# Kernel optimization log

Hardware: AMD Instinct MI355X
Metric: run time of the kernel (lower is better)

Reference implementation:

```python
import jax, jax.numpy as jnp
import numpy as np


def postorder_positions(depth):
    """Post-order index of each node in a perfect binary tree of given depth.
    Returns dict: level -> np.array of post-order indices for the left-to-right
    nodes at that level (level 0 = leaves, level `depth` = root)."""
    levels = {0: np.array([0], dtype=np.int64)}
    size = 1  # size of depth-(d-1) subtree
    for d in range(1, depth + 1):
        new = {l: np.concatenate([levels[l], levels[l] + size]) for l in range(d)}
        new[d] = np.array([2 * size], dtype=np.int64)
        levels = new
        size = 2 * size + 1
    return levels


def setup_inputs() -> dict:
    key = jax.random.key(0)
    k1, k2, k3, k4, k5, k6 = jax.random.split(key, 6)
    VOCAB, E, LBL, LEAVES = 50000, 100, 2, 131072  # 2**17 leaves
    word_ids = jax.random.randint(k1, (LEAVES,), 0, VOCAB, dtype=jnp.int32)
    emb_table = jax.random.normal(k2, (VOCAB, E), dtype=jnp.float32) * 0.1
    Wl = jax.random.normal(k3, (E, E), dtype=jnp.float32) * 0.1
    bl = jax.random.normal(k4, (E,), dtype=jnp.float32) * 0.1
    Wp = jax.random.normal(k5, (LBL, E), dtype=jnp.float32) * 0.1
    bp = jax.random.normal(k6, (LBL,), dtype=jnp.float32) * 0.1
    return {"word_ids": word_ids, "emb_table": emb_table, "Wl": Wl, "bl": bl, "Wp": Wp, "bp": bp}


def reference(word_ids, emb_table, Wl, bl, Wp, bp):
    # Perfect binary tree, batched level-by-level (same math as the per-node
    # Python recursion in the torch module). NOTE: original uses fcl for BOTH
    # children, so internal node = relu(fcl(left) + fcl(right)).
    L = word_ids.shape[0]
    D = int(round(np.log2(L)))
    pos = postorder_positions(D)
    n_nodes = 2 * L - 1

    h = emb_table[word_ids]  # [L, E] leaf states
    out = jnp.zeros((n_nodes, 1, bp.shape[0]), dtype=h.dtype)
    for lvl in range(D + 1):
        proj = h @ Wp.T + bp                     # [n_lvl, label]
        out = out.at[jnp.asarray(pos[lvl])].set(proj[:, None, :])
        if lvl < D:
            # fcl(left)+fcl(right) = (left+right) @ Wl^T + 2*bl, then relu
            h = jax.nn.relu((h[0::2] + h[1::2]) @ Wl.T + 2.0 * bl)
    return out  # [n_nodes, 1, label] in post-order, matching torch.cat(node_list)
```

## Files before the change

### kernel.cpp

```cpp
#include <hip/hip_runtime.h>

typedef _Float16 h8v __attribute__((ext_vector_type(8)));
typedef float f4v __attribute__((ext_vector_type(4)));

#define RS 136
#define SD 68

__device__ __forceinline__ unsigned pk2f(float a, float b) {
  unsigned short ha = __builtin_bit_cast(unsigned short, (_Float16)a);
  unsigned short hb = __builtin_bit_cast(unsigned short, (_Float16)b);
  return (unsigned)ha | ((unsigned)hb << 16);
}
__device__ __forceinline__ float2 upk(unsigned u) {
  _Float16 lo = __builtin_bit_cast(_Float16, (unsigned short)(u & 0xffffu));
  _Float16 hi = __builtin_bit_cast(_Float16, (unsigned short)(u >> 16));
  return make_float2((float)lo, (float)hi);
}

__global__ void prep_kernel(const float* __restrict__ Wl, const float* __restrict__ emb,
                            const float* __restrict__ Wp, const float* __restrict__ bp,
                            unsigned short* __restrict__ Wlf, unsigned* __restrict__ embh,
                            float2* __restrict__ pw, unsigned* __restrict__ cnts) {
  const long t = (long)blockIdx.x * 256 + threadIdx.x;
  if (t < 400000L) {
    const int w = (int)(t >> 3), q = (int)(t & 7);
    const float4* row4 = (const float4*)(emb + (size_t)w * 100);
    uint2* ed = (uint2*)(embh + (size_t)w * 64);
    float q0 = 0.f, q1 = 0.f;
    #pragma unroll
    for (int m = 0; m < 4; ++m) {
      int j = q + 8 * m;
      if (j < 25) {
        float4 v = row4[j];
        q0 = fmaf(v.x, Wp[4*j], fmaf(v.y, Wp[4*j+1],
             fmaf(v.z, Wp[4*j+2], fmaf(v.w, Wp[4*j+3], q0))));
        q1 = fmaf(v.x, Wp[100+4*j], fmaf(v.y, Wp[100+4*j+1],
             fmaf(v.z, Wp[100+4*j+2], fmaf(v.w, Wp[100+4*j+3], q1))));
        ed[j] = make_uint2(pk2f(v.x, v.y), pk2f(v.z, v.w));
      }
    }
    if (q < 7) ed[25 + q] = make_uint2(0u, 0u);
    q0 += __shfl_xor(q0, 1, 64); q0 += __shfl_xor(q0, 2, 64); q0 += __shfl_xor(q0, 4, 64);
    q1 += __shfl_xor(q1, 1, 64); q1 += __shfl_xor(q1, 2, 64); q1 += __shfl_xor(q1, 4, 64);
    if (q == 0) pw[w] = make_float2(q0 + bp[0], q1 + bp[1]);
  } else {
    long j = t - 400128L;
    if (j >= 0 && j < 128 * 128) {
      int o = (int)(j >> 7), k = (int)(j & 127);
      _Float16 v = (_Float16)0.f;
      if (o < 100 && k < 100) v = (_Float16)Wl[o * 100 + k];
      Wlf[j] = __builtin_bit_cast(unsigned short, v);
    }
    if (blockIdx.x == 1563 && threadIdx.x >= 192 && threadIdx.x < 224)
      cnts[threadIdx.x - 192] = 0u;
  }
}

__device__ __forceinline__ void load_bfrags(
    const unsigned short* __restrict__ Wlf, const float* __restrict__ bl,
    h8v (&B0)[4], h8v (&B1)[4], float& bias0, float& bias1,
    int wave, int quad, int c16) {
  int col0 = wave * 32 + c16;
  int col1 = col0 + 16;
  bias0 = (col0 < 100) ? 2.0f * bl[col0] : 0.f;
  bias1 = (col1 < 100) ? 2.0f * bl[col1] : 0.f;
  const _Float16* w0 = (const _Float16*)Wlf + col0 * 128 + quad * 8;
  const _Float16* w1 = (const _Float16*)Wlf + col1 * 128 + quad * 8;
  B0[0] = *(const h8v*)(w0);      B0[1] = *(const h8v*)(w0 + 32);
  B0[2] = *(const h8v*)(w0 + 64); B0[3] = *(const h8v*)(w0 + 96);
  B1[0] = *(const h8v*)(w1);      B1[1] = *(const h8v*)(w1 + 32);
  B1[2] = *(const h8v*)(w1 + 64); B1[3] = *(const h8v*)(w1 + 96);
}

__device__ __forceinline__ void mfma_level(
    const _Float16* srcE, const _Float16* srcO, bool pairMode,
    _Float16* dstE, _Float16* dstO, int nOut,
    const h8v (&B0)[4], const h8v (&B1)[4], float bias0, float bias1,
    int lane, int wave) {
  const int quad = lane >> 4, c16 = lane & 15;
  const int col0 = wave * 32 + c16, col1 = col0 + 16;
  const int tiles = (nOut + 15) >> 4;
  for (int rt = 0; rt < tiles; ++rt) {
    const int r = rt * 16 + c16;
    const h8v* pe = (const h8v*)(srcE + (size_t)r * RS + quad * 8);
    h8v A0, A1, A2, A3;
    if (pairMode) {
      const h8v* po = (const h8v*)(srcO + (size_t)r * RS + quad * 8);
      A0 = pe[0] + po[0];  A1 = pe[4] + po[4];
      A2 = pe[8] + po[8];  A3 = pe[12] + po[12];
    } else {
      A0 = pe[0]; A1 = pe[4]; A2 = pe[8]; A3 = pe[12];
    }
    f4v a0 = {bias0, bias0, bias0, bias0};
    f4v a1 = {bias1, bias1, bias1, bias1};
    a0 = __builtin_amdgcn_mfma_f32_16x16x32_f16(A0, B0[0], a0, 0, 0, 0);
    a0 = __builtin_amdgcn_mfma_f32_16x16x32_f16(A1, B0[1], a0, 0, 0, 0);
    a0 = __builtin_amdgcn_mfma_f32_16x16x32_f16(A2, B0[2], a0, 0, 0, 0);
    a0 = __builtin_amdgcn_mfma_f32_16x16x32_f16(A3, B0[3], a0, 0, 0, 0);
    a1 = __builtin_amdgcn_mfma_f32_16x16x32_f16(A0, B1[0], a1, 0, 0, 0);
    a1 = __builtin_amdgcn_mfma_f32_16x16x32_f16(A1, B1[1], a1, 0, 0, 0);
    a1 = __builtin_amdgcn_mfma_f32_16x16x32_f16(A2, B1[2], a1, 0, 0, 0);
    a1 = __builtin_amdgcn_mfma_f32_16x16x32_f16(A3, B1[3], a1, 0, 0, 0);
    #pragma unroll
    for (int rg = 0; rg < 4; ++rg) {
      int row = rt * 16 + quad * 4 + rg;
      _Float16* dr = ((row & 1) ? dstO : dstE) + (size_t)(row >> 1) * RS;
      dr[col0] = (_Float16)fmaxf(a0[rg], 0.f);
      dr[col1] = (_Float16)fmaxf(a1[rg], 0.f);
    }
  }
}

__device__ __forceinline__ void proj_rows(
    const _Float16* E, const _Float16* O, int nRows, const float* WpS,
    float bp0, float bp1, int lvl, long gbase, float* __restrict__ out, int tid) {
  if (tid >= nRows) return;
  const unsigned* row = (const unsigned*)((tid & 1) ? O : E) + (size_t)(tid >> 1) * SD;
  float q0 = bp0, q1 = bp1;
  #pragma unroll
  for (int p = 0; p < 25; ++p) {
    uint2 u = ((const uint2*)row)[p];
    float2 a = upk(u.x), b = upk(u.y);
    q0 = fmaf(a.x, WpS[4*p], fmaf(a.y, WpS[4*p+1],
         fmaf(b.x, WpS[4*p+2], fmaf(b.y, WpS[4*p+3], q0))));
    q1 = fmaf(a.x, WpS[128+4*p], fmaf(a.y, WpS[128+4*p+1],
         fmaf(b.x, WpS[128+4*p+2], fmaf(b.y, WpS[128+4*p+3], q1))));
  }
  long g = gbase + tid;
  long pos = ((g + 1) << (lvl + 1)) - 2 - __popc((unsigned)g);
  out[2 * pos] = q0; out[2 * pos + 1] = q1;
}

__device__ void tree_phase(
    const unsigned* __restrict__ src, unsigned* __restrict__ hdst,
    _Float16* Ea, _Float16* Oa, _Float16* Eb, _Float16* Ob,
    const float* WpS, float bp0, float bp1,
    const h8v (&B0)[4], const h8v (&B1)[4], float bias0, float bias1,
    float* __restrict__ out, int firstLvl, int nLvl, int nIn, int finalProj,
    long blk, int tid, int lane, int wave) {
  {
    unsigned* Ed = (unsigned*)Ea; unsigned* Od = (unsigned*)Oa;
    for (int i = tid; i < 64 * 64; i += 256) {
      int r = i >> 6, d = i & 63;
      unsigned val = (r < nIn && d < 50)
          ? __hip_atomic_load(&src[(size_t)r * 50 + d], __ATOMIC_RELAXED,
                              __HIP_MEMORY_SCOPE_AGENT)
          : 0u;
      ((r & 1) ? Od : Ed)[(r >> 1) * SD + d] = val;
    }
    unsigned* Ed2 = (unsigned*)Eb; unsigned* Od2 = (unsigned*)Ob;
    for (int i = tid; i < 32 * 64; i += 256) {
      int r = i >> 6, d = i & 63;
      ((r & 1) ? Od2 : Ed2)[(r >> 1) * SD + d] = 0u;
    }
  }
  __syncthreads();
  _Float16 *sE = Ea, *sO = Oa, *dE = Eb, *dO = Ob;
  int n = nIn >> 1;
  for (int p = 0; p < nLvl; ++p) {
    mfma_level(sE, sO, true, dE, dO, n, B0, B1, bias0, bias1, lane, wave);
    proj_rows(sE, sO, n * 2, WpS, bp0, bp1, firstLvl + p - 1,
              blk * (n * 2), out, tid);
    __syncthreads();
    _Float16* t;
    t = sE; sE = dE; dE = t;
    t = sO; sO = dO; dO = t;
    n >>= 1;
  }
  int R = nIn >> nLvl;
  if (finalProj)
    proj_rows(sE, sO, R, WpS, bp0, bp1, firstLvl + nLvl - 1, blk * R, out, tid);
  if (hdst) {
    for (int i = tid; i < R * 50; i += 256) {
      int r = i / 50, d = i % 50;
      unsigned val = ((const unsigned*)((r & 1) ? sO : sE))[(r >> 1) * SD + d];
      __hip_atomic_store(&hdst[(size_t)blk * R * 50 + i], val,
                         __ATOMIC_RELAXED, __HIP_MEMORY_SCOPE_AGENT);
    }
  }
  __syncthreads();
}

__global__ __launch_bounds__(256, 4) void mega_kernel(
    const int* __restrict__ word_ids, const unsigned* __restrict__ embh,
    const float2* __restrict__ pw,
    const unsigned short* __restrict__ Wlf, const float* __restrict__ bl,
    const float* __restrict__ Wp, const float* __restrict__ bp,
    unsigned* __restrict__ h7g, unsigned* __restrict__ h13g,
    unsigned* __restrict__ cnts, float* __restrict__ out) {
  __shared__ _Float16 S1[64 * RS];
  __shared__ _Float16 Ea[32 * RS], Oa[32 * RS];
  __shared__ float WpS[256];
  __shared__ int claimS;
  _Float16* const Eb = S1;
  _Float16* const Ob = S1 + 16 * RS;

  const int tid = threadIdx.x, lane = tid & 63;
  const int wave = __builtin_amdgcn_readfirstlane(tid >> 6);
  const int quad = lane >> 4, c16 = lane & 15;
  const int blk = blockIdx.x;

  {
    int r = tid >> 7, c = tid & 127;
    WpS[tid] = (c < 100) ? Wp[r * 100 + c] : 0.f;
  }
  const float bp0 = bp[0], bp1 = bp[1];

  const int l = tid >> 1, hh = tid & 1;
  const long gL = (long)blk * 128 + l;
  const int wid = word_ids[gL];
  const uint4* erow = (const uint4*)(embh + (size_t)wid * 64 + hh * 32);
  uint4 w4[8];
  #pragma unroll
  for (int i = 0; i < 8; ++i) w4[i] = erow[i];

  if (hh == 0) {
    float2 p = pw[wid];
    long pos = ((gL + 1) << 1) - 2 - __popc((unsigned)gL);
    out[2 * pos] = p.x; out[2 * pos + 1] = p.y;
  }

  {
    unsigned* S1d = (unsigned*)S1;
    const unsigned* wd = (const unsigned*)w4;
    #pragma unroll
    for (int k = 0; k < 32; ++k) {
      unsigned u = wd[k];
      unsigned us = __shfl_xor(u, 2, 64);
      float2 a = upk(u), b = upk(us);
      unsigned pk = pk2f(a.x + b.x, a.y + b.y);
      if ((tid & 2) == 0) S1d[(size_t)(tid >> 2) * SD + hh * 32 + k] = pk;
    }
  }
  h8v B0[4], B1[4]; float bias0, bias1;
  load_bfrags(Wlf, bl, B0, B1, bias0, bias1, wave, quad, c16);
  __syncthreads();

  mfma_level(S1, nullptr, false, Ea, Oa, 64, B0, B1, bias0, bias1, lane, wave);
  __syncthreads();
  mfma_level(Ea, Oa, true, Eb, Ob, 32, B0, B1, bias0, bias1, lane, wave);
  proj_rows(Ea, Oa, 64, WpS, bp0, bp1, 1, (long)blk * 64, out, tid);
  __syncthreads();
  mfma_level(Eb, Ob, true, Ea, Oa, 16, B0, B1, bias0, bias1, lane, wave);
  proj_rows(Eb, Ob, 32, WpS, bp0, bp1, 2, (long)blk * 32, out, tid);
  __syncthreads();
  mfma_level(Ea, Oa, true, Eb, Ob, 8, B0, B1, bias0, bias1, lane, wave);
  proj_rows(Ea, Oa, 16, WpS, bp0, bp1, 3, (long)blk * 16, out, tid);
  __syncthreads();
  mfma_level(Eb, Ob, true, Ea, Oa, 4, B0, B1, bias0, bias1, lane, wave);
  proj_rows(Eb, Ob, 8, WpS, bp0, bp1, 4, (long)blk * 8, out, tid);
  __syncthreads();
  mfma_level(Ea, Oa, true, Eb, Ob, 2, B0, B1, bias0, bias1, lane, wave);
  proj_rows(Ea, Oa, 4, WpS, bp0, bp1, 5, (long)blk * 4, out, tid);
  __syncthreads();
  mfma_level(Eb, Ob, true, Ea, Oa, 1, B0, B1, bias0, bias1, lane, wave);
  proj_rows(Eb, Ob, 2, WpS, bp0, bp1, 6, (long)blk * 2, out, tid);
  __syncthreads();
  if (tid < 50)
    __hip_atomic_store(&h7g[(size_t)blk * 50 + tid], ((unsigned*)Ea)[tid],
                       __ATOMIC_RELAXED, __HIP_MEMORY_SCOPE_AGENT);
  __syncthreads();

  const int g = blk >> 6;
  if (tid == 0) {
    unsigned old = __hip_atomic_fetch_add(&cnts[g], 1u, __ATOMIC_RELAXED,
                                          __HIP_MEMORY_SCOPE_AGENT);
    claimS = (old == 63u);
  }
  __syncthreads();
  if (!claimS) return;

  tree_phase(h7g + (size_t)g * 64 * 50, h13g, Ea, Oa, Eb, Ob, WpS, bp0, bp1,
             B0, B1, bias0, bias1, out, 8, 6, 64, 0, (long)g, tid, lane, wave);

  if (tid == 0) {
    unsigned old = __hip_atomic_fetch_add(&cnts[16], 1u, __ATOMIC_RELAXED,
                                          __HIP_MEMORY_SCOPE_AGENT);
    claimS = (old == 15u);
  }
  __syncthreads();
  if (!claimS) return;

  tree_phase(h13g, nullptr, Ea, Oa, Eb, Ob, WpS, bp0, bp1,
             B0, B1, bias0, bias1, out, 14, 4, 16, 1, 0L, tid, lane, wave);
}

extern "C" void kernel_launch(void* const* d_in, const int* in_sizes, int n_in,
                              void* d_out, int out_size, void* d_ws, size_t ws_size,
                              hipStream_t stream) {
  const int*   word_ids = (const int*)  d_in[0];
  const float* emb      = (const float*)d_in[1];
  const float* Wl       = (const float*)d_in[2];
  const float* bl       = (const float*)d_in[3];
  const float* Wp       = (const float*)d_in[4];
  const float* bp       = (const float*)d_in[5];
  float* out = (float*)d_out;

  unsigned*       embh = (unsigned*)d_ws;
  float2*         pw   = (float2*)((char*)d_ws + 12800000);
  unsigned short* Wlf  = (unsigned short*)((char*)d_ws + 13200000);
  unsigned*       h7g  = (unsigned*)((char*)d_ws + 13232768);
  unsigned*       h13g = (unsigned*)((char*)d_ws + 13437568);
  unsigned*       cnts = (unsigned*)((char*)d_ws + 13440768);

  prep_kernel<<<1627, 256, 0, stream>>>(Wl, emb, Wp, bp, Wlf, embh, pw, cnts);
  mega_kernel<<<1024, 256, 0, stream>>>(word_ids, embh, pw, Wlf, bl, Wp, bp,
                                        h7g, h13g, cnts, out);
}
```

Measured before the change: 145.4 us.

## Halve per-block leaves, shrink LDS row stride, double grid and occupancy

Each block now handles 64 leaves instead of 128, and the grid doubles to 2048 blocks. The fp16 row stride in shared memory drops from 136 to 104 halves, the embedding table stride from 64 to 56 dwords, and the Wp shared copy is removed in favour of direct global reads. Together these cut LDS per block enough for launch bounds of 8 blocks per CU, aiming to raise occupancy and latency hiding. The cross-block reduction tree is rebalanced to match: 32 groups of 64, then a final phase of 32 inputs over 5 levels. The cost is more counter atomics, and proj_rows now reads Wp from global or cache instead of LDS.

```diff
diff --git a/kernel.cpp b/kernel.cpp
--- a/kernel.cpp
+++ b/kernel.cpp
@@ -3,8 +3,10 @@
 typedef _Float16 h8v __attribute__((ext_vector_type(8)));
 typedef float f4v __attribute__((ext_vector_type(4)));
 
-#define RS 136
-#define SD 68
+#define RS 104
+#define SD 52
+#define LROWS 96
+#define LDS_DW (LROWS * SD + 16)
 
 __device__ __forceinline__ unsigned pk2f(float a, float b) {
   unsigned short ha = __builtin_bit_cast(unsigned short, (_Float16)a);
@@ -25,7 +27,7 @@
   if (t < 400000L) {
     const int w = (int)(t >> 3), q = (int)(t & 7);
     const float4* row4 = (const float4*)(emb + (size_t)w * 100);
-    uint2* ed = (uint2*)(embh + (size_t)w * 64);
+    uint2* ed = (uint2*)(embh + (size_t)w * 56);
     float q0 = 0.f, q1 = 0.f;
     #pragma unroll
     for (int m = 0; m < 4; ++m) {
@@ -39,7 +41,7 @@
         ed[j] = make_uint2(pk2f(v.x, v.y), pk2f(v.z, v.w));
       }
     }
-    if (q < 7) ed[25 + q] = make_uint2(0u, 0u);
+    if (q < 3) ed[25 + q] = make_uint2(0u, 0u);
     q0 += __shfl_xor(q0, 1, 64); q0 += __shfl_xor(q0, 2, 64); q0 += __shfl_xor(q0, 4, 64);
     q1 += __shfl_xor(q1, 1, 64); q1 += __shfl_xor(q1, 2, 64); q1 += __shfl_xor(q1, 4, 64);
     if (q == 0) pw[w] = make_float2(q0 + bp[0], q1 + bp[1]);
@@ -51,7 +53,7 @@
       if (o < 100 && k < 100) v = (_Float16)Wl[o * 100 + k];
       Wlf[j] = __builtin_bit_cast(unsigned short, v);
     }
-    if (blockIdx.x == 1563 && threadIdx.x >= 192 && threadIdx.x < 224)
+    if (blockIdx.x == 1563 && threadIdx.x >= 192 && threadIdx.x < 240)
       cnts[threadIdx.x - 192] = 0u;
   }
 }
@@ -105,14 +107,14 @@
     for (int rg = 0; rg < 4; ++rg) {
       int row = rt * 16 + quad * 4 + rg;
       _Float16* dr = ((row & 1) ? dstO : dstE) + (size_t)(row >> 1) * RS;
-      dr[col0] = (_Float16)fmaxf(a0[rg], 0.f);
-      dr[col1] = (_Float16)fmaxf(a1[rg], 0.f);
+      if (col0 < 104) dr[col0] = (_Float16)fmaxf(a0[rg], 0.f);
+      if (col1 < 104) dr[col1] = (_Float16)fmaxf(a1[rg], 0.f);
     }
   }
 }
 
 __device__ __forceinline__ void proj_rows(
-    const _Float16* E, const _Float16* O, int nRows, const float* WpS,
+    const _Float16* E, const _Float16* O, int nRows, const float* __restrict__ Wp,
     float bp0, float bp1, int lvl, long gbase, float* __restrict__ out, int tid) {
   if (tid >= nRows) return;
   const unsigned* row = (const unsigned*)((tid & 1) ? O : E) + (size_t)(tid >> 1) * SD;
@@ -121,10 +123,10 @@
   for (int p = 0; p < 25; ++p) {
     uint2 u = ((const uint2*)row)[p];
     float2 a = upk(u.x), b = upk(u.y);
-    q0 = fmaf(a.x, WpS[4*p], fmaf(a.y, WpS[4*p+1],
-         fmaf(b.x, WpS[4*p+2], fmaf(b.y, WpS[4*p+3], q0))));
-    q1 = fmaf(a.x, WpS[128+4*p], fmaf(a.y, WpS[128+4*p+1],
-         fmaf(b.x, WpS[128+4*p+2], fmaf(b.y, WpS[128+4*p+3], q1))));
+    q0 = fmaf(a.x, Wp[4*p], fmaf(a.y, Wp[4*p+1],
+         fmaf(b.x, Wp[4*p+2], fmaf(b.y, Wp[4*p+3], q0))));
+    q1 = fmaf(a.x, Wp[100+4*p], fmaf(a.y, Wp[100+4*p+1],
+         fmaf(b.x, Wp[100+4*p+2], fmaf(b.y, Wp[100+4*p+3], q1))));
   }
   long g = gbase + tid;
   long pos = ((g + 1) << (lvl + 1)) - 2 - __popc((unsigned)g);
@@ -133,34 +135,34 @@
 
 __device__ void tree_phase(
     const unsigned* __restrict__ src, unsigned* __restrict__ hdst,
-    _Float16* Ea, _Float16* Oa, _Float16* Eb, _Float16* Ob,
-    const float* WpS, float bp0, float bp1,
+    _Float16* TE, _Float16* TO, _Float16* Eb, _Float16* Ob,
+    const float* __restrict__ Wp, float bp0, float bp1,
     const h8v (&B0)[4], const h8v (&B1)[4], float bias0, float bias1,
     float* __restrict__ out, int firstLvl, int nLvl, int nIn, int finalProj,
-    long blk, int tid, int lane, int wave) {
+    long blkg, int tid, int lane, int wave) {
   {
-    unsigned* Ed = (unsigned*)Ea; unsigned* Od = (unsigned*)Oa;
-    for (int i = tid; i < 64 * 64; i += 256) {
-      int r = i >> 6, d = i & 63;
-      unsigned val = (r < nIn && d < 50)
-          ? __hip_atomic_load(&src[(size_t)r * 50 + d], __ATOMIC_RELAXED,
-                              __HIP_MEMORY_SCOPE_AGENT)
-          : 0u;
-      ((r & 1) ? Od : Ed)[(r >> 1) * SD + d] = val;
-    }
-    unsigned* Ed2 = (unsigned*)Eb; unsigned* Od2 = (unsigned*)Ob;
-    for (int i = tid; i < 32 * 64; i += 256) {
-      int r = i >> 6, d = i & 63;
-      ((r & 1) ? Od2 : Ed2)[(r >> 1) * SD + d] = 0u;
-    }
-  }
-  __syncthreads();
-  _Float16 *sE = Ea, *sO = Oa, *dE = Eb, *dO = Ob;
+    unsigned* Ed = (unsigned*)TE; unsigned* Od = (unsigned*)TO;
+    const int d = tid & 63;
+    if (d < SD) {
+      for (int r = tid >> 6; r < 64; r += 4) {
+        unsigned val = 0u;
+        if (r < nIn && d < 50)
+          val = __hip_atomic_load(&src[(size_t)r * 50 + d], __ATOMIC_RELAXED,
+                                  __HIP_MEMORY_SCOPE_AGENT);
+        ((r & 1) ? Od : Ed)[(r >> 1) * SD + d] = val;
+      }
+      unsigned* Ed2 = (unsigned*)Eb; unsigned* Od2 = (unsigned*)Ob;
+      for (int r = tid >> 6; r < 32; r += 4)
+        ((r & 1) ? Od2 : Ed2)[(r >> 1) * SD + d] = 0u;
+    }
+  }
+  __syncthreads();
+  _Float16 *sE = TE, *sO = TO, *dE = Eb, *dO = Ob;
   int n = nIn >> 1;
   for (int p = 0; p < nLvl; ++p) {
     mfma_level(sE, sO, true, dE, dO, n, B0, B1, bias0, bias1, lane, wave);
-    proj_rows(sE, sO, n * 2, WpS, bp0, bp1, firstLvl + p - 1,
-              blk * (n * 2), out, tid);
+    proj_rows(sE, sO, n * 2, Wp, bp0, bp1, firstLvl + p - 1,
+              blkg * (n * 2), out, tid);
     __syncthreads();
     _Float16* t;
     t = sE; sE = dE; dE = t;
@@ -169,95 +171,104 @@
   }
   int R = nIn >> nLvl;
   if (finalProj)
-    proj_rows(sE, sO, R, WpS, bp0, bp1, firstLvl + nLvl - 1, blk * R, out, tid);
+    proj_rows(sE, sO, R, Wp, bp0, bp1, firstLvl + nLvl - 1, blkg * R, out, tid);
   if (hdst) {
     for (int i = tid; i < R * 50; i += 256) {
-      int r = i / 50, d = i % 50;
-      unsigned val = ((const unsigned*)((r & 1) ? sO : sE))[(r >> 1) * SD + d];
-      __hip_atomic_store(&hdst[(size_t)blk * R * 50 + i], val,
+      int r = i / 50, d2 = i % 50;
+      unsigned val = ((const unsigned*)((r & 1) ? sO : sE))[(r >> 1) * SD + d2];
+      __hip_atomic_store(&hdst[(size_t)blkg * R * 50 + i], val,
                          __ATOMIC_RELAXED, __HIP_MEMORY_SCOPE_AGENT);
     }
   }
   __syncthreads();
 }
 
-__global__ __launch_bounds__(256, 4) void mega_kernel(
+__global__ __launch_bounds__(256, 8) void mega_kernel(
     const int* __restrict__ word_ids, const unsigned* __restrict__ embh,
     const float2* __restrict__ pw,
     const unsigned short* __restrict__ Wlf, const float* __restrict__ bl,
     const float* __restrict__ Wp, const float* __restrict__ bp,
-    unsigned* __restrict__ h7g, unsigned* __restrict__ h13g,
+    unsigned* __restrict__ h6g, unsigned* __restrict__ h12g,
     unsigned* __restrict__ cnts, float* __restrict__ out) {
-  __shared__ _Float16 S1[64 * RS];
-  __shared__ _Float16 Ea[32 * RS], Oa[32 * RS];
-  __shared__ float WpS[256];
+  __shared__ _Float16 LB[2 * LDS_DW];
   __shared__ int claimS;
-  _Float16* const Eb = S1;
-  _Float16* const Ob = S1 + 16 * RS;
+  _Float16* const S1 = LB;
+  _Float16* const Ea = LB + 32 * RS;
+  _Float16* const Oa = LB + 48 * RS;
+  _Float16* const Eb = LB + 64 * RS;
+  _Float16* const Ob = LB + 80 * RS;
 
   const int tid = threadIdx.x, lane = tid & 63;
   const int wave = __builtin_amdgcn_readfirstlane(tid >> 6);
   const int quad = lane >> 4, c16 = lane & 15;
   const int blk = blockIdx.x;
 
+  const int l4 = tid >> 2, q = tid & 3;
+  const int wid = word_ids[(size_t)blk * 64 + l4];
+  const uint4* erow = (const uint4*)(embh + (size_t)wid * 56);
+  uint4 w4[4];
+  #pragma unroll
+  for (int k = 0; k < 4; ++k) {
+    int c = q + 4 * k;
+    if (c < 14) w4[k] = erow[c];
+  }
+  float2 p0 = make_float2(0.f, 0.f);
+  if (tid < 64) p0 = pw[word_ids[(size_t)blk * 64 + tid]];
+  const float bp0 = bp[0], bp1 = bp[1];
+
   {
-    int r = tid >> 7, c = tid & 127;
-    WpS[tid] = (c < 100) ? Wp[r * 100 + c] : 0.f;
-  }
-  const float bp0 = bp[0], bp1 = bp[1];
-
-  const int l = tid >> 1, hh = tid & 1;
-  const long gL = (long)blk * 128 + l;
-  const int wid = word_ids[gL];
-  const uint4* erow = (const uint4*)(embh + (size_t)wid * 64 + hh * 32);
-  uint4 w4[8];
-  #pragma unroll
-  for (int i = 0; i < 8; ++i) w4[i] = erow[i];
-
-  if (hh == 0) {
-    float2 p = pw[wid];
-    long pos = ((gL + 1) << 1) - 2 - __popc((unsigned)gL);
-    out[2 * pos] = p.x; out[2 * pos + 1] = p.y;
-  }
+    unsigned* lb = (unsigned*)LB;
+    for (int i = tid; i < LDS_DW; i += 256) lb[i] = 0u;
+  }
+  __syncthreads();
 
   {
     unsigned* S1d = (unsigned*)S1;
-    const unsigned* wd = (const unsigned*)w4;
+    const int m = tid >> 3;
     #pragma unroll
-    for (int k = 0; k < 32; ++k) {
-      unsigned u = wd[k];
-      unsigned us = __shfl_xor(u, 2, 64);
-      float2 a = upk(u), b = upk(us);
-      unsigned pk = pk2f(a.x + b.x, a.y + b.y);
-      if ((tid & 2) == 0) S1d[(size_t)(tid >> 2) * SD + hh * 32 + k] = pk;
+    for (int k = 0; k < 4; ++k) {
+      int c = q + 4 * k;
+      if (c < 14) {
+        uint4 u = w4[k], s;
+        s.x = __shfl_xor(u.x, 4, 64); s.y = __shfl_xor(u.y, 4, 64);
+        s.z = __shfl_xor(u.z, 4, 64); s.w = __shfl_xor(u.w, 4, 64);
+        h8v hm = __builtin_bit_cast(h8v, u);
+        h8v hs = __builtin_bit_cast(h8v, s);
+        h8v sum = hm + hs;
+        if ((tid & 4) == 0 && c < 13)
+          *(uint4*)(S1d + (size_t)m * SD + c * 4) = __builtin_bit_cast(uint4, sum);
+      }
     }
   }
   h8v B0[4], B1[4]; float bias0, bias1;
   load_bfrags(Wlf, bl, B0, B1, bias0, bias1, wave, quad, c16);
-  __syncthreads();
-
-  mfma_level(S1, nullptr, false, Ea, Oa, 64, B0, B1, bias0, bias1, lane, wave);
-  __syncthreads();
-  mfma_level(Ea, Oa, true, Eb, Ob, 32, B0, B1, bias0, bias1, lane, wave);
-  proj_rows(Ea, Oa, 64, WpS, bp0, bp1, 1, (long)blk * 64, out, tid);
-  __syncthreads();
-  mfma_level(Eb, Ob, true, Ea, Oa, 16, B0, B1, bias0, bias1, lane, wave);
-  proj_rows(Eb, Ob, 32, WpS, bp0, bp1, 2, (long)blk * 32, out, tid);
-  __syncthreads();
-  mfma_level(Ea, Oa, true, Eb, Ob, 8, B0, B1, bias0, bias1, lane, wave);
-  proj_rows(Ea, Oa, 16, WpS, bp0, bp1, 3, (long)blk * 16, out, tid);
-  __syncthreads();
-  mfma_level(Eb, Ob, true, Ea, Oa, 4, B0, B1, bias0, bias1, lane, wave);
-  proj_rows(Eb, Ob, 8, WpS, bp0, bp1, 4, (long)blk * 8, out, tid);
-  __syncthreads();
-  mfma_level(Ea, Oa, true, Eb, Ob, 2, B0, B1, bias0, bias1, lane, wave);
-  proj_rows(Ea, Oa, 4, WpS, bp0, bp1, 5, (long)blk * 4, out, tid);
-  __syncthreads();
-  mfma_level(Eb, Ob, true, Ea, Oa, 1, B0, B1, bias0, bias1, lane, wave);
-  proj_rows(Eb, Ob, 2, WpS, bp0, bp1, 6, (long)blk * 2, out, tid);
+
+  if (tid < 64) {
+    long gL = (long)blk * 64 + tid;
+    long pos = ((gL + 1) << 1) - 2 - __popc((unsigned)gL);
+    out[2 * pos] = p0.x; out[2 * pos + 1] = p0.y;
+  }
+  __syncthreads();
+
+  mfma_level(S1, nullptr, false, Ea, Oa, 32, B0, B1, bias0, bias1, lane, wave);
+  __syncthreads();
+  mfma_level(Ea, Oa, true, Eb, Ob, 16, B0, B1, bias0, bias1, lane, wave);
+  proj_rows(Ea, Oa, 32, Wp, bp0, bp1, 1, (long)blk * 32, out, tid);
+  __syncthreads();
+  mfma_level(Eb, Ob, true, Ea, Oa, 8, B0, B1, bias0, bias1, lane, wave);
+  proj_rows(Eb, Ob, 16, Wp, bp0, bp1, 2, (long)blk * 16, out, tid);
+  __syncthreads();
+  mfma_level(Ea, Oa, true, Eb, Ob, 4, B0, B1, bias0, bias1, lane, wave);
+  proj_rows(Ea, Oa, 8, Wp, bp0, bp1, 3, (long)blk * 8, out, tid);
+  __syncthreads();
+  mfma_level(Eb, Ob, true, Ea, Oa, 2, B0, B1, bias0, bias1, lane, wave);
+  proj_rows(Eb, Ob, 4, Wp, bp0, bp1, 4, (long)blk * 4, out, tid);
+  __syncthreads();
+  mfma_level(Ea, Oa, true, Eb, Ob, 1, B0, B1, bias0, bias1, lane, wave);
+  proj_rows(Ea, Oa, 2, Wp, bp0, bp1, 5, (long)blk * 2, out, tid);
   __syncthreads();
   if (tid < 50)
-    __hip_atomic_store(&h7g[(size_t)blk * 50 + tid], ((unsigned*)Ea)[tid],
+    __hip_atomic_store(&h6g[(size_t)blk * 50 + tid], ((unsigned*)Eb)[tid],
                        __ATOMIC_RELAXED, __HIP_MEMORY_SCOPE_AGENT);
   __syncthreads();
 
@@ -270,19 +281,19 @@
   __syncthreads();
   if (!claimS) return;
 
-  tree_phase(h7g + (size_t)g * 64 * 50, h13g, Ea, Oa, Eb, Ob, WpS, bp0, bp1,
-             B0, B1, bias0, bias1, out, 8, 6, 64, 0, (long)g, tid, lane, wave);
+  tree_phase(h6g + (size_t)g * 64 * 50, h12g, S1, Ea, Eb, Ob, Wp, bp0, bp1,
+             B0, B1, bias0, bias1, out, 7, 6, 64, 0, (long)g, tid, lane, wave);
 
   if (tid == 0) {
-    unsigned old = __hip_atomic_fetch_add(&cnts[16], 1u, __ATOMIC_RELAXED,
+    unsigned old = __hip_atomic_fetch_add(&cnts[32], 1u, __ATOMIC_RELAXED,
                                           __HIP_MEMORY_SCOPE_AGENT);
-    claimS = (old == 15u);
+    claimS = (old == 31u);
   }
   __syncthreads();
   if (!claimS) return;
 
-  tree_phase(h13g, nullptr, Ea, Oa, Eb, Ob, WpS, bp0, bp1,
-             B0, B1, bias0, bias1, out, 14, 4, 16, 1, 0L, tid, lane, wave);
+  tree_phase(h12g, nullptr, S1, Ea, Eb, Ob, Wp, bp0, bp1,
+             B0, B1, bias0, bias1, out, 13, 5, 32, 1, 0L, tid, lane, wave);
 }
 
 extern "C" void kernel_launch(void* const* d_in, const int* in_sizes, int n_in,
@@ -297,13 +308,13 @@
   float* out = (float*)d_out;
 
   unsigned*       embh = (unsigned*)d_ws;
-  float2*         pw   = (float2*)((char*)d_ws + 12800000);
-  unsigned short* Wlf  = (unsigned short*)((char*)d_ws + 13200000);
-  unsigned*       h7g  = (unsigned*)((char*)d_ws + 13232768);
-  unsigned*       h13g = (unsigned*)((char*)d_ws + 13437568);
-  unsigned*       cnts = (unsigned*)((char*)d_ws + 13440768);
+  float2*         pw   = (float2*)((char*)d_ws + 11200000);
+  unsigned short* Wlf  = (unsigned short*)((char*)d_ws + 11600000);
+  unsigned*       h6g  = (unsigned*)((char*)d_ws + 11632768);
+  unsigned*       h12g = (unsigned*)((char*)d_ws + 12042368);
+  unsigned*       cnts = (unsigned*)((char*)d_ws + 12048768);
 
   prep_kernel<<<1627, 256, 0, stream>>>(Wl, emb, Wp, bp, Wlf, embh, pw, cnts);
-  mega_kernel<<<1024, 256, 0, stream>>>(word_ids, embh, pw, Wlf, bl, Wp, bp,
-                                        h7g, h13g, cnts, out);
-}
+  mega_kernel<<<2048, 256, 0, stream>>>(word_ids, embh, pw, Wlf, bl, Wp, bp,
+                                        h6g, h12g, cnts, out);
+}
```

Result: slower. 193.3 us (+32.9%).
